# Performance work log

Measured on AMD Instinct MI355X. Metric: run time of the kernel, lower is better.

## Reference

```python
import jax, jax.numpy as jnp
import numpy as np

N_NODES = 100000
N_EDGES = 1600000
HIDDEN = 128
ETYPE_DIM = 16
N_ETYPES = 512
TEMP = 1.0
EPS = 1e-8


def setup_inputs() -> dict:
    key = jax.random.key(0)
    ks = jax.random.split(key, 9)
    d_in = HIDDEN * 2 + ETYPE_DIM  # 272
    return {
        "x": jax.random.normal(ks[0], (N_NODES, HIDDEN), dtype=jnp.float32),
        "edge_index": jax.random.randint(ks[1], (2, N_EDGES), 0, N_NODES),
        "edge_type": jax.random.randint(ks[2], (N_EDGES,), 0, N_ETYPES),
        "u": jax.random.uniform(ks[3], (N_EDGES,), dtype=jnp.float32),
        "etype_emb": jax.random.normal(ks[4], (N_ETYPES, ETYPE_DIM), dtype=jnp.float32),
        "W1": jax.random.normal(ks[5], (d_in, HIDDEN), dtype=jnp.float32) / np.sqrt(d_in),
        "b1": jnp.zeros((HIDDEN,), dtype=jnp.float32),
        "W2": jax.random.normal(ks[6], (HIDDEN, 1), dtype=jnp.float32) / np.sqrt(HIDDEN),
        "b2": jnp.zeros((1,), dtype=jnp.float32),
    }


def reference(x, edge_index, edge_type, u, etype_emb, W1, b1, W2, b2):
    src, dst = edge_index[0], edge_index[1]
    # gather src/dst node embeddings + edge-type embedding, concat -> [E, 2H+D]
    h = jnp.concatenate([x[src], x[dst], etype_emb[edge_type]], axis=-1)
    h = jax.nn.relu(h @ W1 + b1)           # [E, H]
    logits = (h @ W2 + b2).reshape(-1)      # [E]
    # straight-through Gumbel-sigmoid
    g = jnp.log(u + EPS) - jnp.log(1.0 - u + EPS)
    y = jax.nn.sigmoid((logits + g) / max(TEMP, 1e-6))
    y_hard = (y > 0.5).astype(y.dtype)
    y_st = jax.lax.stop_gradient(y_hard - y) + y
    return jnp.stack([logits, y, y_st])  # [3, E]
```

## Files before the change

### kernel.cpp

```cpp
#include <hip/hip_runtime.h>
#include <hip/hip_bf16.h>
#include <math.h>

#define HIDDEN 128
#define EPS_G 1e-8f

__global__ __launch_bounds__(256) void etype_proj_kernel(
    const float* __restrict__ ee, const float* __restrict__ W1,
    const float* __restrict__ b1, float* __restrict__ PetB, int n_etypes)
{
    int gid = blockIdx.x * 256 + threadIdx.x;
    int t = gid >> 7;
    int c = gid & 127;
    if (t >= n_etypes) return;
    float acc = b1[c];
    #pragma unroll
    for (int k = 0; k < 16; ++k) {
        acc = fmaf(ee[t * 16 + k], W1[(256 + k) * 128 + c], acc);
    }
    PetB[t * 128 + c] = acc;
}

#define BM 64
#define BK 32
#define BN 128
#define APAD 36

__global__ __launch_bounds__(256) void node_proj_kernel(
    const float* __restrict__ x, const float* __restrict__ W1,
    float* __restrict__ P, int n_nodes)
{
    __shared__ float As[BM * APAD];
    __shared__ float Bs[BK * BN];

    const int tid  = threadIdx.x;
    const int m0   = blockIdx.x * BM;
    const int half = blockIdx.y;
    const int tm   = tid >> 5;
    const int tn   = tid & 31;

    float acc[8][4];
    #pragma unroll
    for (int i = 0; i < 8; ++i)
        #pragma unroll
        for (int j = 0; j < 4; ++j) acc[i][j] = 0.f;

    const float* Wbase = W1 + (size_t)half * 128 * 128;

    for (int kc = 0; kc < 128; kc += BK) {
        #pragma unroll
        for (int i = 0; i < 2; ++i) {
            int l   = tid + i * 256;
            int row = l >> 3;
            int c4  = (l & 7) << 2;
            int gr  = m0 + row;
            if (gr >= n_nodes) gr = n_nodes - 1;
            float4 v = *(const float4*)(x + (size_t)gr * 128 + kc + c4);
            *(float4*)(&As[row * APAD + c4]) = v;
        }
        #pragma unroll
        for (int i = 0; i < 4; ++i) {
            int l   = tid + i * 256;
            int row = l >> 5;
            int c4  = (l & 31) << 2;
            float4 v = *(const float4*)(Wbase + (size_t)(kc + row) * 128 + c4);
            *(float4*)(&Bs[row * BN + c4]) = v;
        }
        __syncthreads();

        #pragma unroll 8
        for (int kk = 0; kk < BK; ++kk) {
            float a[8];
            #pragma unroll
            for (int i = 0; i < 8; ++i) a[i] = As[(tm * 8 + i) * APAD + kk];
            float4 b = *(const float4*)(&Bs[kk * BN + tn * 4]);
            #pragma unroll
            for (int i = 0; i < 8; ++i) {
                acc[i][0] = fmaf(a[i], b.x, acc[i][0]);
                acc[i][1] = fmaf(a[i], b.y, acc[i][1]);
                acc[i][2] = fmaf(a[i], b.z, acc[i][2]);
                acc[i][3] = fmaf(a[i], b.w, acc[i][3]);
            }
        }
        __syncthreads();
    }

    #pragma unroll
    for (int i = 0; i < 8; ++i) {
        int gr = m0 + tm * 8 + i;
        if (gr < n_nodes) {
            float4 v = make_float4(acc[i][0], acc[i][1], acc[i][2], acc[i][3]);
            *(float4*)(P + (size_t)gr * 256 + half * 128 + tn * 4) = v;
        }
    }
}

__global__ __launch_bounds__(256) void edge_kernel(
    const int* __restrict__ ei, const int* __restrict__ et,
    const float* __restrict__ u, const float* __restrict__ P,
    const float* __restrict__ PetB, const float* __restrict__ W2,
    const float* __restrict__ b2, float* __restrict__ out, int E)
{
    int gtid = blockIdx.x * 256 + threadIdx.x;
    int e = gtid >> 4;
    int l = gtid & 15;
    if (e >= E) return;

    int src = ei[e];
    int dst = ei[E + e];
    int t   = et[e];
    float uu = u[e];

    const float4* ps = (const float4*)(P + (size_t)src * 256);
    const float4* pd = (const float4*)(P + (size_t)dst * 256 + 128);
    const float4* pe = (const float4*)(PetB + (size_t)t * 128);
    const float4* w2 = (const float4*)W2;

    float partial = 0.f;
    #pragma unroll
    for (int j = 0; j < 2; ++j) {
        int idx = l * 2 + j;
        float4 a = ps[idx];
        float4 b = pd[idx];
        float4 c = pe[idx];
        float4 w = w2[idx];
        float h0 = fmaxf(a.x + b.x + c.x, 0.f);
        float h1 = fmaxf(a.y + b.y + c.y, 0.f);
        float h2 = fmaxf(a.z + b.z + c.z, 0.f);
        float h3 = fmaxf(a.w + b.w + c.w, 0.f);
        partial = fmaf(h0, w.x, partial);
        partial = fmaf(h1, w.y, partial);
        partial = fmaf(h2, w.z, partial);
        partial = fmaf(h3, w.w, partial);
    }
    partial += __shfl_xor(partial, 1);
    partial += __shfl_xor(partial, 2);
    partial += __shfl_xor(partial, 4);
    partial += __shfl_xor(partial, 8);

    if (l == 0) {
        float logit = partial + b2[0];
        float g  = logf(uu + EPS_G) - logf(1.f - uu + EPS_G);
        float z  = logit + g;
        float yv = 1.f / (1.f + expf(-z));
        float yh = yv > 0.5f ? 1.f : 0.f;
        float yst = (yh - yv) + yv;
        out[e]         = logit;
        out[E + e]     = yv;
        out[2 * E + e] = yst;
    }
}

__global__ __launch_bounds__(256) void edge_direct_kernel(
    const float* __restrict__ x, const int* __restrict__ ei,
    const int* __restrict__ et, const float* __restrict__ u,
    const float* __restrict__ ee, const float* __restrict__ W1,
    const float* __restrict__ b1, const float* __restrict__ W2,
    const float* __restrict__ b2, float* __restrict__ out, int E)
{
    int wid  = (blockIdx.x * 256 + threadIdx.x) >> 6;
    int lane = threadIdx.x & 63;
    if (wid >= E) return;
    int src = ei[wid], dst = ei[E + wid], t = et[wid];
    int c0 = lane * 2;
    float acc0 = b1[c0], acc1 = b1[c0 + 1];
    for (int k = 0; k < 128; ++k) {
        float xs = x[(size_t)src * 128 + k];
        acc0 = fmaf(xs, W1[k * 128 + c0], acc0);
        acc1 = fmaf(xs, W1[k * 128 + c0 + 1], acc1);
    }
    for (int k = 0; k < 128; ++k) {
        float xd = x[(size_t)dst * 128 + k];
        acc0 = fmaf(xd, W1[(128 + k) * 128 + c0], acc0);
        acc1 = fmaf(xd, W1[(128 + k) * 128 + c0 + 1], acc1);
    }
    for (int k = 0; k < 16; ++k) {
        float ev = ee[t * 16 + k];
        acc0 = fmaf(ev, W1[(256 + k) * 128 + c0], acc0);
        acc1 = fmaf(ev, W1[(256 + k) * 128 + c0 + 1], acc1);
    }
    float partial = fmaxf(acc0, 0.f) * W2[c0] + fmaxf(acc1, 0.f) * W2[c0 + 1];
    #pragma unroll
    for (int off = 1; off < 64; off <<= 1) partial += __shfl_xor(partial, off);
    if (lane == 0) {
        float logit = partial + b2[0];
        float uu = u[wid];
        float g  = logf(uu + EPS_G) - logf(1.f - uu + EPS_G);
        float z  = logit + g;
        float yv = 1.f / (1.f + expf(-z));
        float yh = yv > 0.5f ? 1.f : 0.f;
        float yst = (yh - yv) + yv;
        out[wid]         = logit;
        out[E + wid]     = yv;
        out[2 * E + wid] = yst;
    }
}

extern "C" void kernel_launch(void* const* d_in, const int* in_sizes, int n_in,
                              void* d_out, int out_size, void* d_ws, size_t ws_size,
                              hipStream_t stream)
{
    const float* x   = (const float*)d_in[0];
    const int*   ei  = (const int*)d_in[1];
    const int*   et  = (const int*)d_in[2];
    const float* u   = (const float*)d_in[3];
    const float* ee  = (const float*)d_in[4];
    const float* W1  = (const float*)d_in[5];
    const float* b1  = (const float*)d_in[6];
    const float* W2  = (const float*)d_in[7];
    const float* b2  = (const float*)d_in[8];
    float* out = (float*)d_out;

    const int n_nodes  = in_sizes[0] / HIDDEN;
    const int E        = in_sizes[2];
    const int n_etypes = in_sizes[4] / 16;

    const size_t needP   = (size_t)n_nodes * 256 * sizeof(float);
    const size_t needPet = (size_t)n_etypes * 128 * sizeof(float);

    if (ws_size >= needP + needPet) {
        float* P    = (float*)d_ws;
        float* PetB = (float*)((char*)d_ws + needP);

        hipLaunchKernelGGL(etype_proj_kernel,
                           dim3((n_etypes * 128 + 255) / 256), dim3(256), 0, stream,
                           ee, W1, b1, PetB, n_etypes);
        hipLaunchKernelGGL(node_proj_kernel,
                           dim3((n_nodes + BM - 1) / BM, 2), dim3(256), 0, stream,
                           x, W1, P, n_nodes);
        hipLaunchKernelGGL(edge_kernel,
                           dim3(((size_t)E * 16 + 255) / 256), dim3(256), 0, stream,
                           ei, et, u, P, PetB, W2, b2, out, E);
    } else {
        hipLaunchKernelGGL(edge_direct_kernel,
                           dim3((E + 3) / 4), dim3(256), 0, stream,
                           x, ei, et, u, ee, W1, b1, W2, b2, out, E);
    }
}
```

Measured before the change: 407.7 us.

## Compute both node projection halves per block with transposed A tile

The node projection GEMM now gives each block a full 256-column output (both the src and dst halves of W1) instead of launching two blocks along y, so each x tile is loaded once and reused for both halves. The A tile is stored transposed in shared memory so each thread reads its 8 rows with two float4 loads instead of eight scalar loads. Each thread now holds 64 accumulators, which raises register pressure and may lower occupancy. The edge kernel, which probably dominates runtime, is unchanged.

Result: slower. 417.1 us (+2.3%).

```diff
diff --git a/kernel.cpp b/kernel.cpp
--- a/kernel.cpp
+++ b/kernel.cpp
@@ -15,71 +15,77 @@
     if (t >= n_etypes) return;
     float acc = b1[c];
     #pragma unroll
-    for (int k = 0; k < 16; ++k) {
+    for (int k = 0; k < 16; ++k)
         acc = fmaf(ee[t * 16 + k], W1[(256 + k) * 128 + c], acc);
-    }
     PetB[t * 128 + c] = acc;
 }
 
 #define BM 64
 #define BK 32
-#define BN 128
-#define APAD 36
+#define BNN 256
+#define ASTR 68
 
 __global__ __launch_bounds__(256) void node_proj_kernel(
     const float* __restrict__ x, const float* __restrict__ W1,
     float* __restrict__ P, int n_nodes)
 {
-    __shared__ float As[BM * APAD];
-    __shared__ float Bs[BK * BN];
-
-    const int tid  = threadIdx.x;
-    const int m0   = blockIdx.x * BM;
-    const int half = blockIdx.y;
-    const int tm   = tid >> 5;
-    const int tn   = tid & 31;
-
-    float acc[8][4];
+    __shared__ float As[BK * ASTR];
+    __shared__ float Bs[BK * BNN];
+
+    const int tid = threadIdx.x;
+    const int m0  = blockIdx.x * BM;
+    const int tm  = tid >> 5;
+    const int tn  = tid & 31;
+
+    float acc[8][8];
     #pragma unroll
     for (int i = 0; i < 8; ++i)
         #pragma unroll
-        for (int j = 0; j < 4; ++j) acc[i][j] = 0.f;
-
-    const float* Wbase = W1 + (size_t)half * 128 * 128;
+        for (int j = 0; j < 8; ++j) acc[i][j] = 0.f;
 
     for (int kc = 0; kc < 128; kc += BK) {
         #pragma unroll
         for (int i = 0; i < 2; ++i) {
             int l   = tid + i * 256;
             int row = l >> 3;
-            int c4  = (l & 7) << 2;
+            int k4  = (l & 7) << 2;
             int gr  = m0 + row;
             if (gr >= n_nodes) gr = n_nodes - 1;
-            float4 v = *(const float4*)(x + (size_t)gr * 128 + kc + c4);
-            *(float4*)(&As[row * APAD + c4]) = v;
+            float4 v = *(const float4*)(x + (size_t)gr * 128 + kc + k4);
+            As[(k4 + 0) * ASTR + row] = v.x;
+            As[(k4 + 1) * ASTR + row] = v.y;
+            As[(k4 + 2) * ASTR + row] = v.z;
+            As[(k4 + 3) * ASTR + row] = v.w;
         }
         #pragma unroll
-        for (int i = 0; i < 4; ++i) {
+        for (int i = 0; i < 8; ++i) {
             int l   = tid + i * 256;
-            int row = l >> 5;
-            int c4  = (l & 31) << 2;
-            float4 v = *(const float4*)(Wbase + (size_t)(kc + row) * 128 + c4);
-            *(float4*)(&Bs[row * BN + c4]) = v;
+            int row = l >> 6;
+            int c4  = (l & 63) << 2;
+            const float* sp = (c4 < 128)
+                ? (W1 + (size_t)(kc + row) * 128 + c4)
+                : (W1 + (size_t)(128 + kc + row) * 128 + (c4 - 128));
+            *(float4*)&Bs[row * BNN + c4] = *(const float4*)sp;
         }
         __syncthreads();
 
-        #pragma unroll 8
+        #pragma unroll 4
         for (int kk = 0; kk < BK; ++kk) {
-            float a[8];
-            #pragma unroll
-            for (int i = 0; i < 8; ++i) a[i] = As[(tm * 8 + i) * APAD + kk];
-            float4 b = *(const float4*)(&Bs[kk * BN + tn * 4]);
+            float4 a0  = *(const float4*)&As[kk * ASTR + tm * 8];
+            float4 a1  = *(const float4*)&As[kk * ASTR + tm * 8 + 4];
+            float4 b0  = *(const float4*)&Bs[kk * BNN + tn * 4];
+            float4 b1v = *(const float4*)&Bs[kk * BNN + 128 + tn * 4];
+            float a[8] = {a0.x, a0.y, a0.z, a0.w, a1.x, a1.y, a1.z, a1.w};
             #pragma unroll
             for (int i = 0; i < 8; ++i) {
-                acc[i][0] = fmaf(a[i], b.x, acc[i][0]);
-                acc[i][1] = fmaf(a[i], b.y, acc[i][1]);
-                acc[i][2] = fmaf(a[i], b.z, acc[i][2]);
-                acc[i][3] = fmaf(a[i], b.w, acc[i][3]);
+                acc[i][0] = fmaf(a[i], b0.x,  acc[i][0]);
+                acc[i][1] = fmaf(a[i], b0.y,  acc[i][1]);
+                acc[i][2] = fmaf(a[i], b0.z,  acc[i][2]);
+                acc[i][3] = fmaf(a[i], b0.w,  acc[i][3]);
+                acc[i][4] = fmaf(a[i], b1v.x, acc[i][4]);
+                acc[i][5] = fmaf(a[i], b1v.y, acc[i][5]);
+                acc[i][6] = fmaf(a[i], b1v.z, acc[i][6]);
+                acc[i][7] = fmaf(a[i], b1v.w, acc[i][7]);
             }
         }
         __syncthreads();
@@ -89,8 +95,10 @@
     for (int i = 0; i < 8; ++i) {
         int gr = m0 + tm * 8 + i;
         if (gr < n_nodes) {
-            float4 v = make_float4(acc[i][0], acc[i][1], acc[i][2], acc[i][3]);
-            *(float4*)(P + (size_t)gr * 256 + half * 128 + tn * 4) = v;
+            float4 w0 = make_float4(acc[i][0], acc[i][1], acc[i][2], acc[i][3]);
+            float4 w1 = make_float4(acc[i][4], acc[i][5], acc[i][6], acc[i][7]);
+            *(float4*)(P + (size_t)gr * 256 + tn * 4)       = w0;
+            *(float4*)(P + (size_t)gr * 256 + 128 + tn * 4) = w1;
         }
     }
 }
@@ -226,10 +234,10 @@
                            dim3((n_etypes * 128 + 255) / 256), dim3(256), 0, stream,
                            ee, W1, b1, PetB, n_etypes);
         hipLaunchKernelGGL(node_proj_kernel,
-                           dim3((n_nodes + BM - 1) / BM, 2), dim3(256), 0, stream,
+                           dim3((n_nodes + BM - 1) / BM), dim3(256), 0, stream,
                            x, W1, P, n_nodes);
         hipLaunchKernelGGL(edge_kernel,
-                           dim3(((size_t)E * 16 + 255) / 256), dim3(256), 0, stream,
+                           dim3((int)(((size_t)E * 16 + 255) / 256)), dim3(256), 0, stream,
                            ei, et, u, P, PetB, W2, b2, out, E);
     } else {
         hipLaunchKernelGGL(edge_direct_kernel,
```
